# Performance work log

Measured on AMD Instinct MI355X. Metric: run time of the kernel, lower is better.

Reference implementation:

```python
import jax, jax.numpy as jnp
import numpy as np

B, N, D = 4096, 64, 512
LN_EPS = 1e-5


def setup_inputs() -> dict:
    key = jax.random.key(0)
    k1, k2 = jax.random.split(key)
    return {
        "embeddings": jax.random.normal(k1, (B, N, D), dtype=jnp.float32),
        "ln_gamma": jnp.ones((D,), dtype=jnp.float32),
        "ln_beta": jnp.zeros((D,), dtype=jnp.float32),
        "Wv": jax.random.normal(k2, (D, 1), dtype=jnp.float32) * (1.0 / np.sqrt(D)),
        "bv": jnp.zeros((1,), dtype=jnp.float32),
    }


def reference(embeddings, ln_gamma, ln_beta, Wv, bv):
    # LayerNorm over last dim
    mu = jnp.mean(embeddings, axis=-1, keepdims=True)
    var = jnp.mean(jnp.square(embeddings - mu), axis=-1, keepdims=True)
    e = (embeddings - mu) * jax.lax.rsqrt(var + LN_EPS) * ln_gamma + ln_beta

    query = e[:, :1, :]          # [B, 1, D]
    key_v = e[:, 1:, :]          # [B, N-1, D] (key == value)

    qk = jnp.tanh(query * key_v)                 # broadcasted elementwise mul + tanh
    scores = (qk @ Wv + bv)[..., 0]              # [B, N-1] tiny D->1 projection
    alphas = jax.nn.softmax(scores, axis=-1)[..., None]  # [B, N-1, 1]

    em_a = alphas * key_v                        # softmax-weighted values
    return jnp.concatenate([query, em_a], axis=-2)  # [B, N, D]
```

## Files before the change

### kernel.cpp

```cpp
#include <hip/hip_runtime.h>
#include <math.h>

#define NROWS 64
#define DCOLS 512
#define HCOL  256
#define BDIM  512
#define NWV   8
#define RPW   8

typedef float f32x4 __attribute__((ext_vector_type(4)));
typedef unsigned short u16x4 __attribute__((ext_vector_type(4)));

__device__ __forceinline__ void wave_reduce_sum2(float& a, float& b) {
#pragma unroll
    for (int off = 32; off > 0; off >>= 1) {
        a += __shfl_xor(a, off, 64);
        b += __shfl_xor(b, off, 64);
    }
}
__device__ __forceinline__ float wave_reduce_sum(float v) {
#pragma unroll
    for (int off = 32; off > 0; off >>= 1)
        v += __shfl_xor(v, off, 64);
    return v;
}

__device__ __forceinline__ float hsum8(f32x4 a, f32x4 b) {
    return ((a.x + a.y) + (a.z + a.w)) + ((b.x + b.y) + (b.z + b.w));
}
__device__ __forceinline__ float hsumsq8(f32x4 a, f32x4 b) {
    return (a.x*a.x + a.y*a.y + a.z*a.z + a.w*a.w)
         + (b.x*b.x + b.y*b.y + b.z*b.z + b.w*b.w);
}

__device__ __forceinline__ float fast_tanh(float x) {
    float e = __expf(2.0f * x);
    return 1.0f - 2.0f / (e + 1.0f);
}

__device__ __forceinline__ unsigned short f2b(float f) {
    union { float f; unsigned int u; } v; v.f = f;
    unsigned int r = (v.u + 0x7FFFu + ((v.u >> 16) & 1u)) >> 16;
    return (unsigned short)r;
}
__device__ __forceinline__ float b2f(unsigned short h) {
    union { unsigned int u; float f; } v; v.u = ((unsigned int)h) << 16;
    return v.f;
}

__device__ __forceinline__ void lds_barrier() {
    asm volatile("s_waitcnt lgkmcnt(0)" ::: "memory");
    __builtin_amdgcn_s_barrier();
}

__global__ __launch_bounds__(BDIM, 4) void fused_ln_attn_kernel(
    const float* __restrict__ emb,
    const float* __restrict__ gamma,
    const float* __restrict__ beta,
    const float* __restrict__ Wv,
    const float* __restrict__ bv,
    float* __restrict__ out)
{
    __shared__ unsigned short      s_e1[NROWS * HCOL];
    __shared__ __align__(16) float s_q[DCOLS];
    __shared__ __align__(16) float s_g[DCOLS];
    __shared__ __align__(16) float s_b[DCOLS];
    __shared__ unsigned short      s_w[DCOLS];
    __shared__ float s_den[NWV];

    const int tid  = threadIdx.x;
    const int wave = tid >> 6;
    const int lane = tid & 63;
    const int c0   = lane << 2;
    const int c1   = HCOL + c0;
    const int r0   = wave * RPW;

    s_g[tid] = gamma[tid];
    s_b[tid] = beta[tid];
    s_w[tid] = f2b(Wv[tid]);
    const float bias = bv[0];

    const size_t base = (size_t)blockIdx.x * (size_t)(NROWS * DCOLS);
    const float* eb = emb + base;
    float*       ob = out + base;

    lds_barrier();

    f32x4 e0[RPW];
    {
        const f32x4 g0 = *(const f32x4*)(s_g + c0);
        const f32x4 g1 = *(const f32x4*)(s_g + c1);
        const f32x4 b0 = *(const f32x4*)(s_b + c0);
        const f32x4 b1 = *(const f32x4*)(s_b + c1);
#pragma unroll
        for (int i = 0; i < RPW; ++i) {
            const int r = r0 + i;
            const f32x4 x0 = *(const f32x4*)(eb + r * DCOLS + c0);
            const f32x4 x1 = *(const f32x4*)(eb + r * DCOLS + c1);

            float s = hsum8(x0, x1), ss = hsumsq8(x0, x1);
            wave_reduce_sum2(s, ss);

            const float mu  = s * (1.0f / (float)DCOLS);
            const float var = ss * (1.0f / (float)DCOLS) - mu * mu;
            const float rs  = rsqrtf(var + 1e-5f);

            e0[i] = (x0 - mu) * rs * g0 + b0;
            const f32x4 t1 = (x1 - mu) * rs * g1 + b1;

            u16x4 p;
            p.x = f2b(t1.x); p.y = f2b(t1.y); p.z = f2b(t1.z); p.w = f2b(t1.w);
            *(u16x4*)(s_e1 + r * HCOL + c0) = p;

            if (wave == 0 && i == 0) {
                *(f32x4*)(s_q + c0) = e0[0];
                *(f32x4*)(s_q + c1) = t1;
                __builtin_nontemporal_store(e0[0], (f32x4*)(ob + c0));
                __builtin_nontemporal_store(t1,    (f32x4*)(ob + c1));
            }
        }
    }

    lds_barrier();

    const f32x4 q0 = *(const f32x4*)(s_q + c0);
    const f32x4 q1 = *(const f32x4*)(s_q + c1);
    f32x4 w0, w1;
    {
        const u16x4 wa = *(const u16x4*)(s_w + c0);
        const u16x4 wb = *(const u16x4*)(s_w + c1);
        w0.x = b2f(wa.x); w0.y = b2f(wa.y); w0.z = b2f(wa.z); w0.w = b2f(wa.w);
        w1.x = b2f(wb.x); w1.y = b2f(wb.y); w1.z = b2f(wb.z); w1.w = b2f(wb.w);
    }

    float ex[RPW];
    float denw = 0.0f;
#pragma unroll
    for (int i = 0; i < RPW; ++i) {
        const int r = r0 + i;
        const u16x4 pe = *(const u16x4*)(s_e1 + r * HCOL + c0);
        f32x4 e1;
        e1.x = b2f(pe.x); e1.y = b2f(pe.y); e1.z = b2f(pe.z); e1.w = b2f(pe.w);
        float p;
        p  = fast_tanh(q0.x * e0[i].x) * w0.x;
        p += fast_tanh(q0.y * e0[i].y) * w0.y;
        p += fast_tanh(q0.z * e0[i].z) * w0.z;
        p += fast_tanh(q0.w * e0[i].w) * w0.w;
        p += fast_tanh(q1.x * e1.x) * w1.x;
        p += fast_tanh(q1.y * e1.y) * w1.y;
        p += fast_tanh(q1.z * e1.z) * w1.z;
        p += fast_tanh(q1.w * e1.w) * w1.w;
        const float tot = wave_reduce_sum(p) + bias;
        const float e   = __expf(tot);
        ex[i] = (r == 0) ? 0.0f : e;
        denw += ex[i];
    }
    if (lane == 0) s_den[wave] = denw;

    lds_barrier();

    float den = 0.0f;
#pragma unroll
    for (int w = 0; w < NWV; ++w) den += s_den[w];
    const float inv = 1.0f / den;

#pragma unroll
    for (int i = 0; i < RPW; ++i) {
        const int r = r0 + i;
        if (r == 0) continue;
        const float a = ex[i] * inv;
        const u16x4 pe = *(const u16x4*)(s_e1 + r * HCOL + c0);
        f32x4 e1;
        e1.x = b2f(pe.x); e1.y = b2f(pe.y); e1.z = b2f(pe.z); e1.w = b2f(pe.w);
        __builtin_nontemporal_store(e0[i] * a, (f32x4*)(ob + r * DCOLS + c0));
        __builtin_nontemporal_store(e1 * a,    (f32x4*)(ob + r * DCOLS + c1));
    }
}

extern "C" void kernel_launch(void* const* d_in, const int* in_sizes, int n_in,
                              void* d_out, int out_size, void* d_ws, size_t ws_size,
                              hipStream_t stream) {
    const float* emb   = (const float*)d_in[0];
    const float* gamma = (const float*)d_in[1];
    const float* beta  = (const float*)d_in[2];
    const float* Wv    = (const float*)d_in[3];
    const float* bv    = (const float*)d_in[4];
    float* out = (float*)d_out;

    const int B = in_sizes[0] / (NROWS * DCOLS);
    fused_ln_attn_kernel<<<B, BDIM, 0, stream>>>(emb, gamma, beta, Wv, bv, out);
}
```

Measured before the change: 220.0 us.

## Recompute query LayerNorm per wave to drop a barrier and fuse LN with scoring

Every wave now loads row 0 and computes the query LayerNorm itself, so the shared-memory query buffer and one block barrier go away. LayerNorm and the tanh scoring run in a single loop, and the second half of each row is used directly in fp32 instead of being read back from bf16 LDS. Launch bounds are raised from 4 to 6 waves per SIMD to allow more resident blocks, which puts more pressure on registers. The cost is redundant query-row loads and reductions in every wave.

```diff
diff --git a/kernel.cpp b/kernel.cpp
--- a/kernel.cpp
+++ b/kernel.cpp
@@ -53,7 +53,7 @@
     __builtin_amdgcn_s_barrier();
 }
 
-__global__ __launch_bounds__(BDIM, 4) void fused_ln_attn_kernel(
+__global__ __launch_bounds__(BDIM, 6) void fused_ln_attn_kernel(
     const float* __restrict__ emb,
     const float* __restrict__ gamma,
     const float* __restrict__ beta,
@@ -62,7 +62,6 @@
     float* __restrict__ out)
 {
     __shared__ unsigned short      s_e1[NROWS * HCOL];
-    __shared__ __align__(16) float s_q[DCOLS];
     __shared__ __align__(16) float s_g[DCOLS];
     __shared__ __align__(16) float s_b[DCOLS];
     __shared__ unsigned short      s_w[DCOLS];
@@ -84,47 +83,15 @@
     const float* eb = emb + base;
     float*       ob = out + base;
 
-    lds_barrier();
-
-    f32x4 e0[RPW];
-    {
-        const f32x4 g0 = *(const f32x4*)(s_g + c0);
-        const f32x4 g1 = *(const f32x4*)(s_g + c1);
-        const f32x4 b0 = *(const f32x4*)(s_b + c0);
-        const f32x4 b1 = *(const f32x4*)(s_b + c1);
-#pragma unroll
-        for (int i = 0; i < RPW; ++i) {
-            const int r = r0 + i;
-            const f32x4 x0 = *(const f32x4*)(eb + r * DCOLS + c0);
-            const f32x4 x1 = *(const f32x4*)(eb + r * DCOLS + c1);
-
-            float s = hsum8(x0, x1), ss = hsumsq8(x0, x1);
-            wave_reduce_sum2(s, ss);
-
-            const float mu  = s * (1.0f / (float)DCOLS);
-            const float var = ss * (1.0f / (float)DCOLS) - mu * mu;
-            const float rs  = rsqrtf(var + 1e-5f);
-
-            e0[i] = (x0 - mu) * rs * g0 + b0;
-            const f32x4 t1 = (x1 - mu) * rs * g1 + b1;
-
-            u16x4 p;
-            p.x = f2b(t1.x); p.y = f2b(t1.y); p.z = f2b(t1.z); p.w = f2b(t1.w);
-            *(u16x4*)(s_e1 + r * HCOL + c0) = p;
-
-            if (wave == 0 && i == 0) {
-                *(f32x4*)(s_q + c0) = e0[0];
-                *(f32x4*)(s_q + c1) = t1;
-                __builtin_nontemporal_store(e0[0], (f32x4*)(ob + c0));
-                __builtin_nontemporal_store(t1,    (f32x4*)(ob + c1));
-            }
-        }
-    }
+    const f32x4 qxa = *(const f32x4*)(eb + c0);
+    const f32x4 qxb = *(const f32x4*)(eb + c1);
 
     lds_barrier();
 
-    const f32x4 q0 = *(const f32x4*)(s_q + c0);
-    const f32x4 q1 = *(const f32x4*)(s_q + c1);
+    const f32x4 g0 = *(const f32x4*)(s_g + c0);
+    const f32x4 g1 = *(const f32x4*)(s_g + c1);
+    const f32x4 b0 = *(const f32x4*)(s_b + c0);
+    const f32x4 b1 = *(const f32x4*)(s_b + c1);
     f32x4 w0, w1;
     {
         const u16x4 wa = *(const u16x4*)(s_w + c0);
@@ -133,23 +100,49 @@
         w1.x = b2f(wb.x); w1.y = b2f(wb.y); w1.z = b2f(wb.z); w1.w = b2f(wb.w);
     }
 
+    f32x4 q0, q1;
+    {
+        float s = hsum8(qxa, qxb), ss = hsumsq8(qxa, qxb);
+        wave_reduce_sum2(s, ss);
+        const float mu  = s * (1.0f / (float)DCOLS);
+        const float var = ss * (1.0f / (float)DCOLS) - mu * mu;
+        const float rs  = rsqrtf(var + 1e-5f);
+        q0 = (qxa - mu) * rs * g0 + b0;
+        q1 = (qxb - mu) * rs * g1 + b1;
+    }
+
+    f32x4 e0[RPW];
     float ex[RPW];
     float denw = 0.0f;
 #pragma unroll
     for (int i = 0; i < RPW; ++i) {
         const int r = r0 + i;
-        const u16x4 pe = *(const u16x4*)(s_e1 + r * HCOL + c0);
-        f32x4 e1;
-        e1.x = b2f(pe.x); e1.y = b2f(pe.y); e1.z = b2f(pe.z); e1.w = b2f(pe.w);
+        const f32x4 x0 = *(const f32x4*)(eb + r * DCOLS + c0);
+        const f32x4 x1 = *(const f32x4*)(eb + r * DCOLS + c1);
+
+        float s = hsum8(x0, x1), ss = hsumsq8(x0, x1);
+        wave_reduce_sum2(s, ss);
+
+        const float mu  = s * (1.0f / (float)DCOLS);
+        const float var = ss * (1.0f / (float)DCOLS) - mu * mu;
+        const float rs  = rsqrtf(var + 1e-5f);
+
+        e0[i] = (x0 - mu) * rs * g0 + b0;
+        const f32x4 t1 = (x1 - mu) * rs * g1 + b1;
+
+        u16x4 pk;
+        pk.x = f2b(t1.x); pk.y = f2b(t1.y); pk.z = f2b(t1.z); pk.w = f2b(t1.w);
+        *(u16x4*)(s_e1 + r * HCOL + c0) = pk;
+
         float p;
         p  = fast_tanh(q0.x * e0[i].x) * w0.x;
         p += fast_tanh(q0.y * e0[i].y) * w0.y;
         p += fast_tanh(q0.z * e0[i].z) * w0.z;
         p += fast_tanh(q0.w * e0[i].w) * w0.w;
-        p += fast_tanh(q1.x * e1.x) * w1.x;
-        p += fast_tanh(q1.y * e1.y) * w1.y;
-        p += fast_tanh(q1.z * e1.z) * w1.z;
-        p += fast_tanh(q1.w * e1.w) * w1.w;
+        p += fast_tanh(q1.x * t1.x) * w1.x;
+        p += fast_tanh(q1.y * t1.y) * w1.y;
+        p += fast_tanh(q1.z * t1.z) * w1.z;
+        p += fast_tanh(q1.w * t1.w) * w1.w;
         const float tot = wave_reduce_sum(p) + bias;
         const float e   = __expf(tot);
         ex[i] = (r == 0) ? 0.0f : e;
@@ -167,7 +160,11 @@
 #pragma unroll
     for (int i = 0; i < RPW; ++i) {
         const int r = r0 + i;
-        if (r == 0) continue;
+        if (r == 0) {
+            __builtin_nontemporal_store(q0, (f32x4*)(ob + c0));
+            __builtin_nontemporal_store(q1, (f32x4*)(ob + c1));
+            continue;
+        }
         const float a = ex[i] * inv;
         const u16x4 pe = *(const u16x4*)(s_e1 + r * HCOL + c0);
         f32x4 e1;
```

Measured after the change: 290.2 us. 1.32x slower.
